# Kernel optimization log

Measured on AMD Instinct MI355X. Metric: run time of the kernel, lower is better.

Reference implementation:

```python
import jax, jax.numpy as jnp
import numpy as np

B, S, D = 2, 2048, 1024
H, HD = 16, 64
SCALE = HD ** -0.5  # applied TWICE (q pre-scale + inference score scale), matching the source


def setup_inputs() -> dict:
    key = jax.random.key(0)
    ks = jax.random.split(key, 6)
    std = 0.02
    return {
        "x": jax.random.normal(ks[0], (B, S, D), dtype=jnp.float32),
        "Wq": jax.random.normal(ks[1], (D, D), dtype=jnp.float32) * std,
        "Wk": jax.random.normal(ks[2], (D, D), dtype=jnp.float32) * std,
        "Wv": jax.random.normal(ks[3], (D, D), dtype=jnp.float32) * std,
        "Wo": jax.random.normal(ks[4], (D, D), dtype=jnp.float32) * std,
        "bo": jnp.zeros((D,), dtype=jnp.float32),
    }


def reference(x, Wq, Wk, Wv, Wo, bo):
    b, s, d = x.shape
    # nn.Linear: y = x @ W^T ; split heads: b s (h hd) -> b h s hd
    def split_heads(y):
        return y.reshape(b, s, H, HD).transpose(0, 2, 1, 3)

    q = split_heads(x @ Wq.T) * SCALE          # forward pre-scales q
    k = split_heads(x @ Wk.T)
    v = split_heads(x @ Wv.T)

    # inference path scales scores by SCALE again (double scaling, faithful)
    scores = jnp.einsum("bhsd,bhtd->bhst", q, k) * SCALE  # [B,H,S,S]
    causal = jnp.triu(jnp.full((s, s), -jnp.inf, dtype=scores.dtype), k=1)
    scores = scores + causal[None, None]

    # explicit stable softmax as in the source
    m = jnp.max(scores, axis=-1, keepdims=True)
    e = jnp.exp(scores - m)
    attn = e / jnp.sum(e, axis=-1, keepdims=True)

    out = jnp.einsum("bhst,bhtd->bhsd", attn, v)          # [B,H,S,HD]
    out = out.transpose(0, 2, 1, 3).reshape(b, s, d)       # b h s hd -> b s (h hd)
    return out @ Wo.T + bo
```

## Files before the change

kernel.cpp:

```cpp
#include <hip/hip_runtime.h>
#include <stdint.h>

#define S_LEN 2048
#define DMODEL 1024
#define NHEAD 16
#define HDIM 64
#define BATCH 2

typedef float f32x4 __attribute__((ext_vector_type(4)));
typedef __bf16 bf16x8 __attribute__((ext_vector_type(8)));

typedef const void __attribute__((address_space(1)))* as1_cvp;
typedef void __attribute__((address_space(3)))* as3_vp;

__device__ __forceinline__ ushort f2bf(float f) {
    union { float f; unsigned u; } v; v.f = f;
    unsigned u = v.u;
    return (ushort)((u + 0x7fffu + ((u >> 16) & 1u)) >> 16);
}

__device__ __forceinline__ void gload16(const void* g, void* l) {
    __builtin_amdgcn_global_load_lds((as1_cvp)g, (as3_vp)l, 16, 0, 0);
}

__global__ __launch_bounds__(256) void cvt_all(
    const float* __restrict__ x,  const float* __restrict__ wq,
    const float* __restrict__ wk, const float* __restrict__ wv,
    const float* __restrict__ wo,
    ushort* __restrict__ xb, ushort* __restrict__ wqkv, ushort* __restrict__ wob,
    float qscale) {
    const float* src; ushort* dst; int n; float sc = 1.0f;
    const int DD = DMODEL * DMODEL;
    switch (blockIdx.y) {
        case 0: src = x;  dst = xb;            n = BATCH * S_LEN * DMODEL; break;
        case 1: src = wq; dst = wqkv;          n = DD; sc = qscale; break;
        case 2: src = wk; dst = wqkv + DD;     n = DD; break;
        case 3: src = wv; dst = wqkv + 2 * DD; n = DD; break;
        default: src = wo; dst = wob;          n = DD; break;
    }
    const int step = gridDim.x * 256 * 8;
    for (int i = (blockIdx.x * 256 + threadIdx.x) * 8; i < n; i += step) {
        float4 a = *(const float4*)(src + i);
        float4 b = *(const float4*)(src + i + 4);
        union { ushort us[8]; int4 v; } r;
        r.us[0] = f2bf(a.x * sc); r.us[1] = f2bf(a.y * sc);
        r.us[2] = f2bf(a.z * sc); r.us[3] = f2bf(a.w * sc);
        r.us[4] = f2bf(b.x * sc); r.us[5] = f2bf(b.y * sc);
        r.us[6] = f2bf(b.z * sc); r.us[7] = f2bf(b.w * sc);
        *(int4*)(dst + i) = r.v;
    }
}

template<int BM, int BN, bool F32OUT, bool BIAS>
__global__ __launch_bounds__(256) void gemm_nt(
    const ushort* __restrict__ A, const ushort* __restrict__ B,
    void* __restrict__ Cv, const float* __restrict__ bias,
    int M, int N, int K) {
    __shared__ ushort As[2][BM][32];
    __shared__ ushort Bs[2][BN][32];
    constexpr int MR = BM / 32, NR = BN / 32, AG = BM / 64, BG = BN / 64;
    const int tid = threadIdx.x;
    const int wave = tid >> 6, lane = tid & 63;
    const int wm = (wave >> 1) * (BM / 2), wn = (wave & 1) * (BN / 2);
    const int bm = blockIdx.x * BM, bn = blockIdx.y * BN;
    const int l15 = lane & 15, lg = lane >> 4;
    f32x4 acc[MR][NR] = {};

    const int sr = lane >> 2, sc_ = (lane & 3) * 8;
    const ushort* gA[AG]; const ushort* gB[BG];
    ushort* lA[2][AG]; ushort* lB[2][BG];
#pragma unroll
    for (int i = 0; i < AG; i++) {
        const int r0 = wave * (BM / 4) + i * 16;
        gA[i] = A + (size_t)(bm + r0 + sr) * K + sc_;
        lA[0][i] = &As[0][r0][0]; lA[1][i] = &As[1][r0][0];
    }
#pragma unroll
    for (int i = 0; i < BG; i++) {
        const int r0 = wave * (BN / 4) + i * 16;
        gB[i] = B + (size_t)(bn + r0 + sr) * K + sc_;
        lB[0][i] = &Bs[0][r0][0]; lB[1][i] = &Bs[1][r0][0];
    }

    const int NT = K / 32;
#pragma unroll
    for (int i = 0; i < AG; i++) gload16(gA[i], lA[0][i]);
#pragma unroll
    for (int i = 0; i < BG; i++) gload16(gB[i], lB[0][i]);
    __syncthreads();

    for (int t = 0; t < NT; t++) {
        const int cur = t & 1;
        if (t + 1 < NT) {
            const int off = (t + 1) * 32;
#pragma unroll
            for (int i = 0; i < AG; i++) gload16(gA[i] + off, lA[cur ^ 1][i]);
#pragma unroll
            for (int i = 0; i < BG; i++) gload16(gB[i] + off, lB[cur ^ 1][i]);
        }
        bf16x8 af[MR], bfr[NR];
#pragma unroll
        for (int m = 0; m < MR; m++) {
            int4 t_ = *(const int4*)&As[cur][wm + m * 16 + l15][lg * 8];
            af[m] = __builtin_bit_cast(bf16x8, t_);
        }
#pragma unroll
        for (int n = 0; n < NR; n++) {
            int4 t_ = *(const int4*)&Bs[cur][wn + n * 16 + l15][lg * 8];
            bfr[n] = __builtin_bit_cast(bf16x8, t_);
        }
        __builtin_amdgcn_s_setprio(1);
#pragma unroll
        for (int m = 0; m < MR; m++)
#pragma unroll
            for (int n = 0; n < NR; n++)
                acc[m][n] = __builtin_amdgcn_mfma_f32_16x16x32_bf16(af[m], bfr[n], acc[m][n], 0, 0, 0);
        __builtin_amdgcn_s_setprio(0);
        __syncthreads();
    }

    float* Cf = (float*)Cv;
    ushort* Cb = (ushort*)Cv;
#pragma unroll
    for (int m = 0; m < MR; m++) {
        const int row = bm + wm + m * 16 + lg * 4;
#pragma unroll
        for (int n = 0; n < NR; n++) {
            const int col = bn + wn + n * 16 + l15;
            const float bb = BIAS ? bias[col] : 0.0f;
#pragma unroll
            for (int j = 0; j < 4; j++) {
                float v = acc[m][n][j];
                if (F32OUT) Cf[(size_t)(row + j) * N + col] = v + bb;
                else        Cb[(size_t)(row + j) * N + col] = f2bf(v);
            }
        }
    }
}

__global__ __launch_bounds__(256) void attn_fwd(
    const ushort* __restrict__ QKV, ushort* __restrict__ Og) {
    __shared__ ushort Ks[2][64][72];
    __shared__ ushort Vt[2][64][72];
    __shared__ ushort Ps[4][16][76];
    const int tid = threadIdx.x;
    const int wave = tid >> 6, lane = tid & 63;
    const int l15 = lane & 15, lg = lane >> 4;
    const int a = blockIdx.x;
    const int qtS = a, qtB = 31 - a;
    const int bh = blockIdx.y;
    const int b = bh >> 4, h = bh & 15;
    const ushort* Qb = QKV + (size_t)b * S_LEN * 3072 + h * HDIM;
    const ushort* Kb = Qb + 1024;
    const ushort* Vb = Qb + 2048;

    const int4 onesi = {0x3F803F80, 0x3F803F80, 0x3F803F80, 0x3F803F80};
    const bf16x8 ones = __builtin_bit_cast(bf16x8, onesi);

    bf16x8 qfS[2], qfB[2];
#pragma unroll
    for (int kk = 0; kk < 2; kk++) {
        int4 tS = *(const int4*)(Qb + (size_t)(qtS * 64 + wave * 16 + l15) * 3072 + kk * 32 + lg * 8);
        qfS[kk] = __builtin_bit_cast(bf16x8, tS);
        int4 tB = *(const int4*)(Qb + (size_t)(qtB * 64 + wave * 16 + l15) * 3072 + kk * 32 + lg * 8);
        qfB[kk] = __builtin_bit_cast(bf16x8, tB);
    }

    f32x4 oS[4] = {}, oB[4] = {};
    f32x4 lS = {}, lB = {};

    const int kr = tid >> 2, kc = (tid & 3) * 8;
    const int vt_ = tid & 63, vh = (tid >> 6) * 8;
    int4 kreg0, kreg1, vreg0, vreg1;

    auto LOAD = [&](int t) {
        const ushort* kp = Kb + (size_t)(t * 64 + kr) * 3072 + kc;
        kreg0 = *(const int4*)kp;
        kreg1 = *(const int4*)(kp + 32);
        const ushort* vp = Vb + (size_t)(t * 64 + vt_) * 3072 + vh;
        vreg0 = *(const int4*)vp;
        vreg1 = *(const int4*)(vp + 32);
    };
    auto STORE = [&](int buf) {
        *(int4*)&Ks[buf][kr][kc]      = kreg0;
        *(int4*)&Ks[buf][kr][kc + 32] = kreg1;
        union { int4 v; ushort us[8]; } u0, u1;
        u0.v = vreg0; u1.v = vreg1;
#pragma unroll
        for (int j = 0; j < 8; j++) Vt[buf][vh + j][vt_] = u0.us[j];
#pragma unroll
        for (int j = 0; j < 8; j++) Vt[buf][32 + vh + j][vt_] = u1.us[j];
    };

    auto COMPUTE = [&](const bf16x8 (&qf)[2], f32x4 (&o)[4], f32x4& lacc,
                       bool diag, int cur) {
        f32x4 s[4] = {};
        __builtin_amdgcn_s_setprio(1);
#pragma unroll
        for (int kk = 0; kk < 2; kk++) {
#pragma unroll
            for (int n = 0; n < 4; n++) {
                int4 t = *(const int4*)&Ks[cur][n * 16 + l15][kk * 32 + lg * 8];
                s[n] = __builtin_amdgcn_mfma_f32_16x16x32_bf16(qf[kk], __builtin_bit_cast(bf16x8, t), s[n], 0, 0, 0);
            }
        }
        __builtin_amdgcn_s_setprio(0);
        if (diag) {
            const int qrow = wave * 16 + lg * 4;
#pragma unroll
            for (int n = 0; n < 4; n++) {
                const int tg = n * 16 + l15;
#pragma unroll
                for (int j = 0; j < 4; j++)
                    if (tg > qrow + j) s[n][j] = -1e30f;
            }
        }
#pragma unroll
        for (int n = 0; n < 4; n++)
#pragma unroll
            for (int j = 0; j < 4; j++)
                Ps[wave][lg * 4 + j][n * 16 + l15] = f2bf(__expf(s[n][j]));
        asm volatile("s_waitcnt lgkmcnt(0)" ::: "memory");
        __builtin_amdgcn_s_setprio(1);
#pragma unroll
        for (int kk = 0; kk < 2; kk++) {
            int4 tp = *(const int4*)&Ps[wave][l15][kk * 32 + lg * 8];
            bf16x8 pf = __builtin_bit_cast(bf16x8, tp);
#pragma unroll
            for (int n = 0; n < 4; n++) {
                int4 tv = *(const int4*)&Vt[cur][n * 16 + l15][kk * 32 + lg * 8];
                o[n] = __builtin_amdgcn_mfma_f32_16x16x32_bf16(pf, __builtin_bit_cast(bf16x8, tv), o[n], 0, 0, 0);
            }
            lacc = __builtin_amdgcn_mfma_f32_16x16x32_bf16(pf, ones, lacc, 0, 0, 0);
        }
        __builtin_amdgcn_s_setprio(0);
    };

    LOAD(0);
    STORE(0);
    __syncthreads();

    for (int t0 = 0; t0 <= qtB; ++t0) {
        const int cur = t0 & 1;
        if (t0 < qtB) LOAD(t0 + 1);
        COMPUTE(qfB, oB, lB, t0 == qtB, cur);
        if (t0 <= qtS) COMPUTE(qfS, oS, lS, t0 == qtS, cur);
        if (t0 < qtB) {
            STORE(cur ^ 1);
            __syncthreads();
        }
    }

#pragma unroll
    for (int j = 0; j < 4; j++) { lS[j] = 1.0f / lS[j]; lB[j] = 1.0f / lB[j]; }
#pragma unroll
    for (int n = 0; n < 4; n++)
#pragma unroll
        for (int j = 0; j < 4; j++) {
            const int qrS = qtS * 64 + wave * 16 + lg * 4 + j;
            Og[((size_t)(b * S_LEN + qrS)) * DMODEL + h * HDIM + n * 16 + l15] = f2bf(oS[n][j] * lS[j]);
            const int qrB = qtB * 64 + wave * 16 + lg * 4 + j;
            Og[((size_t)(b * S_LEN + qrB)) * DMODEL + h * HDIM + n * 16 + l15] = f2bf(oB[n][j] * lB[j]);
        }
}

extern "C" void kernel_launch(void* const* d_in, const int* in_sizes, int n_in,
                              void* d_out, int out_size, void* d_ws, size_t ws_size,
                              hipStream_t stream) {
    (void)in_sizes; (void)n_in; (void)out_size; (void)ws_size;
    const float* x  = (const float*)d_in[0];
    const float* Wq = (const float*)d_in[1];
    const float* Wk = (const float*)d_in[2];
    const float* Wv = (const float*)d_in[3];
    const float* Wo = (const float*)d_in[4];
    const float* bo = (const float*)d_in[5];
    float* out = (float*)d_out;

    const int M = BATCH * S_LEN;
    const int D = DMODEL;

    char* ws = (char*)d_ws;
    ushort* xb   = (ushort*)ws; ws += (size_t)M * D * 2;
    ushort* wqkv = (ushort*)ws; ws += (size_t)3 * D * D * 2;
    ushort* wob  = (ushort*)ws; ws += (size_t)D * D * 2;
    ushort* qkvb = (ushort*)ws; ws += (size_t)M * 3 * D * 2;
    ushort* ao   = (ushort*)ws; ws += (size_t)M * D * 2;

    const float qscale = 1.0f / 64.0f;
    cvt_all<<<dim3(512, 5), 256, 0, stream>>>(x, Wq, Wk, Wv, Wo, xb, wqkv, wob, qscale);

    gemm_nt<128, 128, false, false><<<dim3(M / 128, 3 * D / 128), 256, 0, stream>>>(
        xb, wqkv, qkvb, nullptr, M, 3 * D, D);

    attn_fwd<<<dim3(16, BATCH * NHEAD), 256, 0, stream>>>(qkvb, ao);

    gemm_nt<64, 128, true, true><<<dim3(M / 64, D / 128), 256, 0, stream>>>(
        ao, wob, out, bo, M, D, D);
}
```

Before: 200.4 us.

## Triple-buffer GEMM LDS tiles with explicit vmcnt waits and XOR swizzle

Switches the projection GEMM from double to triple buffering, issuing global-to-LDS loads two stages ahead. The __syncthreads is replaced by a partial s_waitcnt vmcnt plus s_barrier, so loads stay in flight across iterations. Source columns are XOR-swizzled to reduce LDS bank conflicts on fragment reads. This uses more LDS, and the hard-coded vmcnt(4) assumes a fixed number of loads per stage, which may not hold for every BM/BN instantiation.

```diff
diff --git a/kernel.cpp b/kernel.cpp
--- a/kernel.cpp
+++ b/kernel.cpp
@@ -56,8 +56,8 @@
     const ushort* __restrict__ A, const ushort* __restrict__ B,
     void* __restrict__ Cv, const float* __restrict__ bias,
     int M, int N, int K) {
-    __shared__ ushort As[2][BM][32];
-    __shared__ ushort Bs[2][BN][32];
+    __shared__ ushort As[3][BM][32];
+    __shared__ ushort Bs[3][BN][32];
     constexpr int MR = BM / 32, NR = BN / 32, AG = BM / 64, BG = BN / 64;
     const int tid = threadIdx.x;
     const int wave = tid >> 6, lane = tid & 63;
@@ -66,47 +66,49 @@
     const int l15 = lane & 15, lg = lane >> 4;
     f32x4 acc[MR][NR] = {};
 
-    const int sr = lane >> 2, sc_ = (lane & 3) * 8;
+    const int sr = lane >> 2;
+    const int ssw = (((lane & 3) ^ ((lane >> 3) & 3))) * 8;
     const ushort* gA[AG]; const ushort* gB[BG];
-    ushort* lA[2][AG]; ushort* lB[2][BG];
+    int rA0[AG], rB0[BG];
 #pragma unroll
     for (int i = 0; i < AG; i++) {
-        const int r0 = wave * (BM / 4) + i * 16;
-        gA[i] = A + (size_t)(bm + r0 + sr) * K + sc_;
-        lA[0][i] = &As[0][r0][0]; lA[1][i] = &As[1][r0][0];
+        rA0[i] = wave * (BM / 4) + i * 16;
+        gA[i] = A + (size_t)(bm + rA0[i] + sr) * K + ssw;
     }
 #pragma unroll
     for (int i = 0; i < BG; i++) {
-        const int r0 = wave * (BN / 4) + i * 16;
-        gB[i] = B + (size_t)(bn + r0 + sr) * K + sc_;
-        lB[0][i] = &Bs[0][r0][0]; lB[1][i] = &Bs[1][r0][0];
+        rB0[i] = wave * (BN / 4) + i * 16;
+        gB[i] = B + (size_t)(bn + rB0[i] + sr) * K + ssw;
     }
 
     const int NT = K / 32;
-#pragma unroll
-    for (int i = 0; i < AG; i++) gload16(gA[i], lA[0][i]);
-#pragma unroll
-    for (int i = 0; i < BG; i++) gload16(gB[i], lB[0][i]);
-    __syncthreads();
-
+    auto STAGE = [&](int t) {
+        const int buf = t % 3;
+        const int off = t * 32;
+#pragma unroll
+        for (int i = 0; i < AG; i++) gload16(gA[i] + off, &As[buf][rA0[i]][0]);
+#pragma unroll
+        for (int i = 0; i < BG; i++) gload16(gB[i] + off, &Bs[buf][rB0[i]][0]);
+    };
+
+    STAGE(0);
+    if (NT > 1) STAGE(1);
+    asm volatile("s_waitcnt vmcnt(4)" ::: "memory");
+    asm volatile("s_barrier" ::: "memory");
+
+    const int csA = (l15 >> 1) & 3;
     for (int t = 0; t < NT; t++) {
-        const int cur = t & 1;
-        if (t + 1 < NT) {
-            const int off = (t + 1) * 32;
-#pragma unroll
-            for (int i = 0; i < AG; i++) gload16(gA[i] + off, lA[cur ^ 1][i]);
-#pragma unroll
-            for (int i = 0; i < BG; i++) gload16(gB[i] + off, lB[cur ^ 1][i]);
-        }
+        const int cur = t % 3;
+        if (t + 2 < NT) STAGE(t + 2);
         bf16x8 af[MR], bfr[NR];
 #pragma unroll
         for (int m = 0; m < MR; m++) {
-            int4 t_ = *(const int4*)&As[cur][wm + m * 16 + l15][lg * 8];
+            int4 t_ = *(const int4*)&As[cur][wm + m * 16 + l15][(lg ^ csA) * 8];
             af[m] = __builtin_bit_cast(bf16x8, t_);
         }
 #pragma unroll
         for (int n = 0; n < NR; n++) {
-            int4 t_ = *(const int4*)&Bs[cur][wn + n * 16 + l15][lg * 8];
+            int4 t_ = *(const int4*)&Bs[cur][wn + n * 16 + l15][(lg ^ csA) * 8];
             bfr[n] = __builtin_bit_cast(bf16x8, t_);
         }
         __builtin_amdgcn_s_setprio(1);
@@ -116,7 +118,11 @@
             for (int n = 0; n < NR; n++)
                 acc[m][n] = __builtin_amdgcn_mfma_f32_16x16x32_bf16(af[m], bfr[n], acc[m][n], 0, 0, 0);
         __builtin_amdgcn_s_setprio(0);
-        __syncthreads();
+        if (t + 1 < NT) {
+            if (t + 2 < NT) asm volatile("s_waitcnt vmcnt(4)" ::: "memory");
+            else            asm volatile("s_waitcnt vmcnt(0)" ::: "memory");
+            asm volatile("s_barrier" ::: "memory");
+        }
     }
 
     float* Cf = (float*)Cv;
```

Measured after the change: 197.4 us. Within noise of the previous version (-1.5%).
